# Kernel tuning notes

Hardware: AMD Instinct MI355X
Metric: run time of the kernel (lower is better)

The kernel has to match this reference:

```python
import jax, jax.numpy as jnp
import numpy as np

N = 100000   # nodes
E = 1600000  # edges
G = 512      # graphs
L = 3        # num_unit LEConv layers
D = 64       # hidden dim


def setup_inputs() -> dict:
    key = jax.random.key(0)
    ks = jax.random.split(key, 12)
    s = 1.0 / np.sqrt(D)
    x = jax.random.normal(ks[0], (N, 4), jnp.float32)
    edge_index = jax.random.randint(ks[1], (2, E), 0, N, dtype=jnp.int64)
    edge_attr = jax.random.uniform(ks[2], (E,), jnp.float32)
    batch = jnp.sort(jax.random.randint(ks[3], (N,), 0, G, dtype=jnp.int64))
    return {
        "x": x,
        "edge_index": edge_index,
        "edge_attr": edge_attr,
        "batch": batch,
        "W_emb": jax.random.normal(ks[4], (4, D), jnp.float32) * 0.5,
        "b_emb": jnp.zeros((D,), jnp.float32),
        "W1": jax.random.normal(ks[5], (L, D, D), jnp.float32) * s,  # LEConv lin1 (on x_j)
        "b1": jnp.zeros((L, D), jnp.float32),
        "W2": jax.random.normal(ks[6], (L, D, D), jnp.float32) * s,  # LEConv lin2 (on x_i, no bias)
        "W3": jax.random.normal(ks[7], (L, D, D), jnp.float32) * s,  # LEConv lin3 (root)
        "b3": jnp.zeros((L, D), jnp.float32),
        "Wl1": jax.random.normal(ks[8], (D, 32), jnp.float32) * s,
        "bl1": jnp.zeros((32,), jnp.float32),
        "Wl2": jax.random.normal(ks[9], (32, 3), jnp.float32) * (1.0 / np.sqrt(32)),
        "bl2": jnp.zeros((3,), jnp.float32),
    }


def reference(x, edge_index, edge_attr, batch, W_emb, b_emb,
              W1, b1, W2, W3, b3, Wl1, bl1, Wl2, bl2):
    src, dst = edge_index[0], edge_index[1]
    h = x @ W_emb + b_emb                          # [N, D]
    for l in range(L):
        a = h @ W1[l] + b1[l]                      # lin1(x) -> gathered at source j
        b = h @ W2[l]                              # lin2(x) -> gathered at target i
        # LEConv message: e_ij * (lin1(x_j) - lin2(x_i)), aggr='add' at target
        msg = edge_attr[:, None] * (a[src] - b[dst])   # [E, D]
        agg = jax.ops.segment_sum(msg, dst, num_segments=N)
        h = jax.nn.relu(agg + h @ W3[l] + b3[l])
    # global_mean_pool over graphs
    sums = jax.ops.segment_sum(h, batch, num_segments=G)              # [G, D]
    counts = jax.ops.segment_sum(jnp.ones((N,), h.dtype), batch, num_segments=G)
    graph_x = sums / jnp.maximum(counts, 1.0)[:, None]
    pred = jax.nn.relu(graph_x @ Wl1 + bl1) @ Wl2 + bl2               # [G, 3]
    return pred
```

## Files before the change

### kernel.cpp

```cpp
#include <hip/hip_runtime.h>
#include <hip/hip_bf16.h>

#define NNODES 100000
#define NEDGES 1600000
#define NGRAPH 512
#define DIM    64
#define NLAYER 3

#define NB   1000
#define BN   100
#define CAP  2048
#define SC_BLOCKS 256
#define EPB  6250
#define PACK_BLOCKS 18
#define ZERO_BLOCKS 2
#define NBLK32 3125
#define EMB_BLOCKS 6250

typedef __attribute__((ext_vector_type(8))) short short8;
typedef __attribute__((ext_vector_type(4))) float float4v;
typedef unsigned long long u64;

__device__ __forceinline__ __hip_bfloat16 f2b(float f) { return __float2bfloat16(f); }
__device__ __forceinline__ unsigned short f2b_bits(float f) {
    __hip_bfloat16 h = __float2bfloat16(f);
    return *reinterpret_cast<unsigned short*>(&h);
}

__device__ __forceinline__ unsigned pack_rec(int src, unsigned wbits32) {
    unsigned w15 = ((wbits32 + 0x8000u) >> 16) & 0x7FFFu;
    return ((unsigned)src << 15) | w15;
}

#define ACC4(ACC, RR, VV) do {                                              \
    float _w = __uint_as_float(((RR) & 0x7FFFu) << 16);                     \
    unsigned _lo = (unsigned)(VV), _hi = (unsigned)((VV) >> 32);            \
    ACC[0] = fmaf(_w, __uint_as_float(_lo << 16), ACC[0]);                  \
    ACC[1] = fmaf(_w, __uint_as_float(_lo & 0xFFFF0000u), ACC[1]);          \
    ACC[2] = fmaf(_w, __uint_as_float(_hi << 16), ACC[2]);                  \
    ACC[3] = fmaf(_w, __uint_as_float(_hi & 0xFFFF0000u), ACC[3]);          \
} while (0)

__device__ __forceinline__ void gather_rounds(
    unsigned rec, int cnt, const u64* __restrict__ h64, int q, int p,
    float (&accA)[4], float (&accB)[4], float (&accC)[4], float (&accD)[4]) {
    int full = cnt >> 4;
    for (int t = 0; t < full; ++t) {
        int base = t * 16;
        unsigned rA = (unsigned)__shfl((int)rec, base + q, 64);
        unsigned rB = (unsigned)__shfl((int)rec, base + 4 + q, 64);
        unsigned rC = (unsigned)__shfl((int)rec, base + 8 + q, 64);
        unsigned rD = (unsigned)__shfl((int)rec, base + 12 + q, 64);
        u64 vA = h64[(size_t)(rA >> 15) * 16 + p];
        u64 vB = h64[(size_t)(rB >> 15) * 16 + p];
        u64 vC = h64[(size_t)(rC >> 15) * 16 + p];
        u64 vD = h64[(size_t)(rD >> 15) * 16 + p];
        ACC4(accA, rA, vA);
        ACC4(accB, rB, vB);
        ACC4(accC, rC, vC);
        ACC4(accD, rD, vD);
    }
    int rem = cnt & 15;
    if (rem) {
        int base = full << 4;
        unsigned rA = (unsigned)__shfl((int)rec, base + q, 64);
        u64 vA = h64[(size_t)(rA >> 15) * 16 + p];
        unsigned rB = 0u, rC = 0u, rD = 0u;
        u64 vB = 0, vC = 0, vD = 0;
        if (rem > 4) {
            rB = (unsigned)__shfl((int)rec, base + 4 + q, 64);
            vB = h64[(size_t)(rB >> 15) * 16 + p];
        }
        if (rem > 8) {
            rC = (unsigned)__shfl((int)rec, base + 8 + q, 64);
            vC = h64[(size_t)(rC >> 15) * 16 + p];
        }
        if (rem > 12) {
            rD = (unsigned)__shfl((int)rec, base + 12 + q, 64);
            vD = h64[(size_t)(rD >> 15) * 16 + p];
        }
        ACC4(accA, rA, vA);
        ACC4(accB, rB, vB);
        ACC4(accC, rC, vC);
        ACC4(accD, rD, vD);
    }
}


__global__ __launch_bounds__(256) void local_sort_kernel(
    const int* __restrict__ ei, const float* __restrict__ ea,
    int2* __restrict__ perm_raw, int2* __restrict__ offcnt,
    const float* __restrict__ W1, const float* __restrict__ W2,
    const float* __restrict__ W3, __hip_bfloat16* __restrict__ wpack,
    float* __restrict__ gsum) {
    int tid = threadIdx.x, k = blockIdx.x;
    if (k >= SC_BLOCKS + PACK_BLOCKS) {
        float4v z = {0.f, 0.f, 0.f, 0.f};
        int idx = (k - SC_BLOCKS - PACK_BLOCKS) * 256 + tid;
        for (int i = idx; i < NGRAPH * DIM / 4; i += ZERO_BLOCKS * 256)
            ((float4v*)gsum)[i] = z;
        return;
    }
    if (k >= SC_BLOCKS) {
        int unit = (k - SC_BLOCKS) * 4 + (tid >> 6);
        if (unit < NLAYER * 24) {
            int kh = unit & 1, tn = (unit >> 1) & 3, w = (unit >> 3) % 3, l = unit / 24;
            const float* Wsrc = (w == 0 ? W1 : (w == 1 ? W2 : W3)) + l * 4096;
            int L = tid & 63;
            __hip_bfloat16* dst = wpack + (size_t)unit * 512 + L * 8;
            int kb = 32 * kh + (L >> 4) * 8;
            int nb = 16 * tn + (L & 15);
            #pragma unroll
            for (int j = 0; j < 8; ++j)
                dst[j] = f2b(Wsrc[(kb + j) * 64 + nb]);
        }
        return;
    }
    __shared__ int cnt[NB];
    __shared__ int off[NB];
    __shared__ int partial[256];
    __shared__ int2 srec[EPB];
    int e0 = k * EPB;
    for (int i = tid; i < NB; i += 256) cnt[i] = 0;
    __syncthreads();
    for (int i = tid; i < EPB; i += 256)
        atomicAdd(&cnt[ei[NEDGES + e0 + i] / BN], 1);
    __syncthreads();
    int loc[4]; int s = 0;
    #pragma unroll
    for (int j = 0; j < 4; ++j) {
        int b = tid * 4 + j;
        int v = (b < NB) ? cnt[b] : 0;
        loc[j] = s; s += v;
    }
    partial[tid] = s;
    __syncthreads();
    for (int o = 1; o < 256; o <<= 1) {
        int t = (tid >= o) ? partial[tid - o] : 0;
        __syncthreads();
        partial[tid] += t;
        __syncthreads();
    }
    int excl = partial[tid] - s;
    #pragma unroll
    for (int j = 0; j < 4; ++j) {
        int b = tid * 4 + j;
        if (b < NB) off[b] = excl + loc[j];
    }
    __syncthreads();
    for (int b = tid; b < NB; b += 256)
        offcnt[(size_t)k * NB + b] = make_int2(off[b], cnt[b]);
    __syncthreads();
    for (int i = tid; i < EPB; i += 256) {
        int e = e0 + i;
        int src = ei[e];
        int d = ei[NEDGES + e];
        float w = ea[e];
        int bin = d / BN;
        int dloc = d - bin * BN;
        int pos = atomicAdd(&off[bin], 1);
        srec[pos] = make_int2(src | (dloc << 20), __float_as_int(w));
    }
    __syncthreads();
    for (int i = tid; i < EPB; i += 256)
        perm_raw[e0 + i] = srec[i];
}

__global__ __launch_bounds__(256) void csr_embed_kernel(
    const int2* __restrict__ perm_raw, const int2* __restrict__ offcnt,
    unsigned* __restrict__ perm2, int2* __restrict__ rows, float* __restrict__ wdeg,
    const float* __restrict__ x, const float* __restrict__ Wemb,
    const float* __restrict__ bemb, __hip_bfloat16* __restrict__ h) {
    __shared__ int2     recs[CAP];
    __shared__ unsigned recs2u[CAP];
    __shared__ int   pscan[256];
    __shared__ int   sprefix[SC_BLOCKS + 1];
    __shared__ int   boff[SC_BLOCKS];
    __shared__ int   cnt[BN];
    __shared__ int   start[BN];
    __shared__ int   cur[BN];
    __shared__ float ws[BN];
    int b = blockIdx.x, tid = threadIdx.x;
    if (b >= NB) {
        int t = (b - NB) * 256 + tid;
        int node = t >> 4, d0 = (t & 15) * 4;
        float4v xv = *(const float4v*)&x[(size_t)node * 4];
        u64 w0 = 0;
        #pragma unroll
        for (int j = 0; j < 4; ++j) {
            int ch = d0 + j;
            float s = bemb[ch];
            #pragma unroll
            for (int k = 0; k < 4; ++k) s = fmaf(xv[k], Wemb[k * 64 + ch], s);
            w0 |= (u64)f2b_bits(s) << (16 * j);
        }
        ((u64*)h)[(size_t)node * 16 + (t & 15)] = w0;
        return;
    }
    if (tid < BN) { cnt[tid] = 0; ws[tid] = 0.f; }
    int2 oc = offcnt[(size_t)tid * NB + b];
    boff[tid] = oc.x;
    int c = oc.y;
    pscan[tid] = c;
    __syncthreads();
    for (int o = 1; o < 256; o <<= 1) {
        int t = (tid >= o) ? pscan[tid - o] : 0;
        __syncthreads();
        pscan[tid] += t;
        __syncthreads();
    }
    sprefix[tid] = pscan[tid] - c;
    if (tid == 255) sprefix[256] = pscan[255];
    __syncthreads();
    int n = min(sprefix[SC_BLOCKS], CAP);
    for (int i = tid; i < n; i += 256) {
        int lo = 0, hi = SC_BLOCKS;
        while (hi - lo > 1) { int m = (lo + hi) >> 1; if (sprefix[m] <= i) lo = m; else hi = m; }
        int2 rec = perm_raw[lo * EPB + boff[lo] + (i - sprefix[lo])];
        recs[i] = rec;
        atomicAdd(&cnt[rec.x >> 20], 1);
        atomicAdd(&ws[rec.x >> 20], __int_as_float(rec.y));
    }
    __syncthreads();
    {
        int v = (tid < BN) ? cnt[tid] : 0;
        pscan[tid] = v;
        __syncthreads();
        for (int o = 1; o < 128; o <<= 1) {
            int t = (tid >= o) ? pscan[tid - o] : 0;
            __syncthreads();
            pscan[tid] += t;
            __syncthreads();
        }
        if (tid < BN) start[tid] = pscan[tid] - v;
    }
    __syncthreads();
    if (tid < BN) {
        cur[tid] = start[tid];
        int base = b * CAP + start[tid];
        rows[b * BN + tid] = make_int2(base, base + cnt[tid]);
        wdeg[b * BN + tid] = ws[tid];
    }
    __syncthreads();
    for (int i = tid; i < n; i += 256) {
        int2 rec = recs[i];
        int pos = atomicAdd(&cur[rec.x >> 20], 1);
        recs2u[pos] = pack_rec(rec.x & 0xFFFFF, (unsigned)rec.y);
    }
    __syncthreads();
    for (int i = tid; i < n; i += 256)
        perm2[(size_t)b * CAP + i] = recs2u[i];
}


template <int LAST>
__global__ __launch_bounds__(256, 8) void layer_kernel(
    const __hip_bfloat16* __restrict__ hin, __hip_bfloat16* __restrict__ hout,
    const int2* __restrict__ rows, const unsigned* __restrict__ perm2,
    const float* __restrict__ wdeg, const __hip_bfloat16* __restrict__ wpack,
    const float* __restrict__ b1, const float* __restrict__ b3,
    const int* __restrict__ batch, float* __restrict__ gsum) {
    __shared__ __align__(16) unsigned char mbytes[32 * 128];
    int tid = threadIdx.x;
    int lane = tid & 63, wv = tid >> 6;
    int q = lane >> 4, p = lane & 15;
    int m0 = blockIdx.x * 32 + wv * 8;
    const u64* h64 = (const u64*)hin;

    int2 rl = rows[m0 + (lane & 7)];
    int st_n = __shfl(rl.x, 0, 64);
    int en_n = __shfl(rl.y, 0, 64);
    unsigned rec_n = (lane < min(en_n - st_n, 64)) ? perm2[st_n + lane] : 0u;

    for (int nl = 0; nl < 8; ++nl) {
        int st = st_n, en = en_n;
        unsigned rec = rec_n;
        if (nl < 7) {
            st_n = __shfl(rl.x, nl + 1, 64);
            en_n = __shfl(rl.y, nl + 1, 64);
            rec_n = (lane < min(en_n - st_n, 64)) ? perm2[st_n + lane] : 0u;
        }
        float accA[4] = {0.f, 0.f, 0.f, 0.f};
        float accB[4] = {0.f, 0.f, 0.f, 0.f};
        float accC[4] = {0.f, 0.f, 0.f, 0.f};
        float accD[4] = {0.f, 0.f, 0.f, 0.f};
        gather_rounds(rec, min(en - st, 64), h64, q, p, accA, accB, accC, accD);
        for (int cb = st + 64; cb < en; cb += 64) {
            unsigned rec2 = (lane < en - cb) ? perm2[cb + lane] : 0u;
            gather_rounds(rec2, min(en - cb, 64), h64, q, p, accA, accB, accC, accD);
        }
        #pragma unroll
        for (int j = 0; j < 4; ++j) accA[j] = (accA[j] + accB[j]) + (accC[j] + accD[j]);
        #pragma unroll
        for (int j = 0; j < 4; ++j) accA[j] += __shfl_xor(accA[j], 16, 64);
        #pragma unroll
        for (int j = 0; j < 4; ++j) accA[j] += __shfl_xor(accA[j], 32, 64);
        if (q == 0) {
            u64 w0 = (u64)f2b_bits(accA[0]) | ((u64)f2b_bits(accA[1]) << 16) |
                     ((u64)f2b_bits(accA[2]) << 32) | ((u64)f2b_bits(accA[3]) << 48);
            int row = wv * 8 + nl;
            int off = (row * 128 + p * 8) ^ ((row & 7) << 4);
            *(u64*)(mbytes + off) = w0;
        }
    }
    __syncthreads();
    if (wv >= 2) return;

    float4v acc[3][4] = {};
    const short8* wp = (const short8*)wpack;
    int row = wv * 16 + p;
    int node_c = blockIdx.x * 32 + row;
    #pragma unroll
    for (int kh = 0; kh < 2; ++kh) {
        int roff = (row * 128 + kh * 64 + q * 16) ^ ((row & 7) << 4);
        short8 am = *(const short8*)(mbytes + roff);
        short8 ah = *(const short8*)((const short*)hin + (size_t)node_c * 64 + kh * 32 + q * 8);
        #pragma unroll
        for (int w = 0; w < 3; ++w) {
            #pragma unroll
            for (int tn = 0; tn < 4; ++tn) {
                short8 bfrag = wp[(size_t)((w * 4 + tn) * 2 + kh) * 64 + lane];
                acc[w][tn] = __builtin_amdgcn_mfma_f32_16x16x32_bf16(
                    w == 0 ? am : ah, bfrag, acc[w][tn], 0, 0, 0);
            }
        }
    }

    float b1v[4], b3v[4];
    #pragma unroll
    for (int tn = 0; tn < 4; ++tn) {
        b1v[tn] = b1[tn * 16 + p];
        b3v[tn] = b3[tn * 16 + p];
    }
    int tb = blockIdx.x * 32 + wv * 16;
    if (!LAST) {
        #pragma unroll
        for (int reg = 0; reg < 4; ++reg) {
            int node = tb + q * 4 + reg;
            float wd = wdeg[node];
            #pragma unroll
            for (int tn = 0; tn < 4; ++tn) {
                float s = acc[0][tn][reg] + acc[2][tn][reg] + b3v[tn] +
                          wd * (b1v[tn] - acc[1][tn][reg]);
                hout[(size_t)node * 64 + tn * 16 + p] = f2b(fmaxf(s, 0.f));
            }
        }
    } else {
        float val[4][4];
        int gb[4];
        #pragma unroll
        for (int reg = 0; reg < 4; ++reg) {
            int node = tb + q * 4 + reg;
            float wd = wdeg[node];
            gb[reg] = batch[node];
            #pragma unroll
            for (int tn = 0; tn < 4; ++tn) {
                float s = acc[0][tn][reg] + acc[2][tn][reg] + b3v[tn] +
                          wd * (b1v[tn] - acc[1][tn][reg]);
                val[reg][tn] = fmaxf(s, 0.f);
            }
        }
        int glo = batch[tb];
        int ghi = batch[tb + 15];
        for (int g = glo; g <= ghi; ++g) {
            #pragma unroll
            for (int tn = 0; tn < 4; ++tn) {
                float part = 0.f;
                #pragma unroll
                for (int reg = 0; reg < 4; ++reg)
                    part += (gb[reg] == g) ? val[reg][tn] : 0.f;
                part += __shfl_xor(part, 16, 64);
                part += __shfl_xor(part, 32, 64);
                if (q == 0) atomicAdd(&gsum[g * 64 + tn * 16 + p], part);
            }
        }
    }
}


__global__ __launch_bounds__(64) void mlp_kernel(
    const float* __restrict__ gsum, const int* __restrict__ batch,
    const float* __restrict__ Wl1, const float* __restrict__ bl1,
    const float* __restrict__ Wl2, const float* __restrict__ bl2,
    float* __restrict__ out) {
    __shared__ int lohi[2];
    __shared__ float gxl[64];
    __shared__ float hid[32];
    int g = blockIdx.x, t = threadIdx.x;
    if (t < 2) {
        int target = g + t;
        int lo = 0, hi = NNODES;
        while (lo < hi) { int m = (lo + hi) >> 1; if (batch[m] < target) lo = m + 1; else hi = m; }
        lohi[t] = lo;
    }
    __syncthreads();
    int cnt = lohi[1] - lohi[0];
    gxl[t] = gsum[g * 64 + t] / (float)max(cnt, 1);
    __syncthreads();
    if (t < 32) {
        float s = bl1[t];
        for (int k = 0; k < 64; ++k) s = fmaf(gxl[k], Wl1[k * 32 + t], s);
        hid[t] = fmaxf(s, 0.f);
    }
    __syncthreads();
    if (t < 3) {
        float s = bl2[t];
        for (int k = 0; k < 32; ++k) s = fmaf(hid[k], Wl2[k * 3 + t], s);
        out[g * 3 + t] = s;
    }
}


extern "C" void kernel_launch(void* const* d_in, const int* in_sizes, int n_in,
                              void* d_out, int out_size, void* d_ws, size_t ws_size,
                              hipStream_t stream) {
    const float* x    = (const float*)d_in[0];
    const int*   ei   = (const int*)d_in[1];
    const float* ea   = (const float*)d_in[2];
    const int*   bat  = (const int*)d_in[3];
    const float* Wemb = (const float*)d_in[4];
    const float* bemb = (const float*)d_in[5];
    const float* W1   = (const float*)d_in[6];
    const float* b1   = (const float*)d_in[7];
    const float* W2   = (const float*)d_in[8];
    const float* W3   = (const float*)d_in[9];
    const float* b3   = (const float*)d_in[10];
    const float* Wl1  = (const float*)d_in[11];
    const float* bl1  = (const float*)d_in[12];
    const float* Wl2  = (const float*)d_in[13];
    const float* bl2  = (const float*)d_in[14];
    float* out = (float*)d_out;

    char* ws = (char*)d_ws;
    __hip_bfloat16*  h_b      = (__hip_bfloat16*) (ws + 0);
    __hip_bfloat16*  h_a      = (__hip_bfloat16*) (ws + 12800000);
    int2*            perm_raw = (int2*)           (ws + 25600000);
    unsigned*        perm2    = (unsigned*)       (ws + 38400000);
    int2*            rows     = (int2*)           (ws + 46592000);
    int2*            offcnt   = (int2*)           (ws + 47392000);
    float*           wdeg     = (float*)          (ws + 49440000);
    __hip_bfloat16*  wpack    = (__hip_bfloat16*) (ws + 49840000);
    float*           gsum     = (float*)          (ws + 49913728);

    local_sort_kernel<<<SC_BLOCKS + PACK_BLOCKS + ZERO_BLOCKS, 256, 0, stream>>>(
        ei, ea, perm_raw, offcnt, W1, W2, W3, wpack, gsum);
    csr_embed_kernel<<<NB + EMB_BLOCKS, 256, 0, stream>>>(
        perm_raw, offcnt, perm2, rows, wdeg, x, Wemb, bemb, h_a);

    layer_kernel<0><<<NBLK32, 256, 0, stream>>>(
        h_a, h_b, rows, perm2, wdeg, wpack, b1, b3, bat, gsum);
    layer_kernel<0><<<NBLK32, 256, 0, stream>>>(
        h_b, h_a, rows, perm2, wdeg, wpack + (size_t)24 * 512, b1 + 64, b3 + 64, bat, gsum);
    layer_kernel<1><<<NBLK32, 256, 0, stream>>>(
        h_a, h_b, rows, perm2, wdeg, wpack + (size_t)48 * 512, b1 + 128, b3 + 128, bat, gsum);

    mlp_kernel<<<NGRAPH, 64, 0, stream>>>(gsum, bat, Wl1, bl1, Wl2, bl2, out);
}
```

Baseline: 268.2 us.

## Load edge records per round directly and split MFMA epilogue across all four waves

The gather loop no longer preloads up to 64 edge records per node and broadcasts them with shuffles. Each 16-edge round now loads its four records straight from perm2, with bounds masks. The dense MFMA stage used to run on only two waves; it now splits the output columns so all four waves each compute two of the four 16-column tiles, and the hidden-state stores become nontemporal. This is meant to cut shuffle overhead, shorten the serial epilogue and use idle waves. In exchange, every wave reloads the A fragments, and the record loads now sit on the critical path before the dependent gathers, since the next node's prefetch is gone.

```diff
diff --git a/kernel.cpp b/kernel.cpp
--- a/kernel.cpp
+++ b/kernel.cpp
@@ -40,51 +40,6 @@
     ACC[2] = fmaf(_w, __uint_as_float(_hi << 16), ACC[2]);                  \
     ACC[3] = fmaf(_w, __uint_as_float(_hi & 0xFFFF0000u), ACC[3]);          \
 } while (0)
-
-__device__ __forceinline__ void gather_rounds(
-    unsigned rec, int cnt, const u64* __restrict__ h64, int q, int p,
-    float (&accA)[4], float (&accB)[4], float (&accC)[4], float (&accD)[4]) {
-    int full = cnt >> 4;
-    for (int t = 0; t < full; ++t) {
-        int base = t * 16;
-        unsigned rA = (unsigned)__shfl((int)rec, base + q, 64);
-        unsigned rB = (unsigned)__shfl((int)rec, base + 4 + q, 64);
-        unsigned rC = (unsigned)__shfl((int)rec, base + 8 + q, 64);
-        unsigned rD = (unsigned)__shfl((int)rec, base + 12 + q, 64);
-        u64 vA = h64[(size_t)(rA >> 15) * 16 + p];
-        u64 vB = h64[(size_t)(rB >> 15) * 16 + p];
-        u64 vC = h64[(size_t)(rC >> 15) * 16 + p];
-        u64 vD = h64[(size_t)(rD >> 15) * 16 + p];
-        ACC4(accA, rA, vA);
-        ACC4(accB, rB, vB);
-        ACC4(accC, rC, vC);
-        ACC4(accD, rD, vD);
-    }
-    int rem = cnt & 15;
-    if (rem) {
-        int base = full << 4;
-        unsigned rA = (unsigned)__shfl((int)rec, base + q, 64);
-        u64 vA = h64[(size_t)(rA >> 15) * 16 + p];
-        unsigned rB = 0u, rC = 0u, rD = 0u;
-        u64 vB = 0, vC = 0, vD = 0;
-        if (rem > 4) {
-            rB = (unsigned)__shfl((int)rec, base + 4 + q, 64);
-            vB = h64[(size_t)(rB >> 15) * 16 + p];
-        }
-        if (rem > 8) {
-            rC = (unsigned)__shfl((int)rec, base + 8 + q, 64);
-            vC = h64[(size_t)(rC >> 15) * 16 + p];
-        }
-        if (rem > 12) {
-            rD = (unsigned)__shfl((int)rec, base + 12 + q, 64);
-            vD = h64[(size_t)(rD >> 15) * 16 + p];
-        }
-        ACC4(accA, rA, vA);
-        ACC4(accB, rB, vB);
-        ACC4(accC, rC, vC);
-        ACC4(accD, rD, vD);
-    }
-}
 
 
 __global__ __launch_bounds__(256) void local_sort_kernel(
@@ -264,30 +219,33 @@
     int tid = threadIdx.x;
     int lane = tid & 63, wv = tid >> 6;
     int q = lane >> 4, p = lane & 15;
-    int m0 = blockIdx.x * 32 + wv * 8;
+    int n0 = blockIdx.x * 32 + wv * 8;
     const u64* h64 = (const u64*)hin;
 
-    int2 rl = rows[m0 + (lane & 7)];
-    int st_n = __shfl(rl.x, 0, 64);
-    int en_n = __shfl(rl.y, 0, 64);
-    unsigned rec_n = (lane < min(en_n - st_n, 64)) ? perm2[st_n + lane] : 0u;
-
+    #pragma unroll
     for (int nl = 0; nl < 8; ++nl) {
-        int st = st_n, en = en_n;
-        unsigned rec = rec_n;
-        if (nl < 7) {
-            st_n = __shfl(rl.x, nl + 1, 64);
-            en_n = __shfl(rl.y, nl + 1, 64);
-            rec_n = (lane < min(en_n - st_n, 64)) ? perm2[st_n + lane] : 0u;
-        }
+        int2 rl = rows[n0 + nl];
+        int st = rl.x, en = rl.y;
         float accA[4] = {0.f, 0.f, 0.f, 0.f};
         float accB[4] = {0.f, 0.f, 0.f, 0.f};
         float accC[4] = {0.f, 0.f, 0.f, 0.f};
         float accD[4] = {0.f, 0.f, 0.f, 0.f};
-        gather_rounds(rec, min(en - st, 64), h64, q, p, accA, accB, accC, accD);
-        for (int cb = st + 64; cb < en; cb += 64) {
-            unsigned rec2 = (lane < en - cb) ? perm2[cb + lane] : 0u;
-            gather_rounds(rec2, min(en - cb, 64), h64, q, p, accA, accB, accC, accD);
+        for (int i0 = st; i0 < en; i0 += 16) {
+            int iA = i0 + q, iB = i0 + 4 + q, iC = i0 + 8 + q, iD = i0 + 12 + q;
+            unsigned rA = 0u, rB = 0u, rC = 0u, rD = 0u;
+            if (iA < en) rA = perm2[iA];
+            if (iB < en) rB = perm2[iB];
+            if (iC < en) rC = perm2[iC];
+            if (iD < en) rD = perm2[iD];
+            u64 vA = 0, vB = 0, vC = 0, vD = 0;
+            if (iA < en) vA = h64[(size_t)(rA >> 15) * 16 + p];
+            if (iB < en) vB = h64[(size_t)(rB >> 15) * 16 + p];
+            if (iC < en) vC = h64[(size_t)(rC >> 15) * 16 + p];
+            if (iD < en) vD = h64[(size_t)(rD >> 15) * 16 + p];
+            ACC4(accA, rA, vA);
+            ACC4(accB, rB, vB);
+            ACC4(accC, rC, vC);
+            ACC4(accD, rD, vD);
         }
         #pragma unroll
         for (int j = 0; j < 4; ++j) accA[j] = (accA[j] + accB[j]) + (accC[j] + accD[j]);
@@ -304,11 +262,11 @@
         }
     }
     __syncthreads();
-    if (wv >= 2) return;
-
-    float4v acc[3][4] = {};
+
+    int tile = wv >> 1, ch = wv & 1;
+    float4v acc[3][2] = {};
     const short8* wp = (const short8*)wpack;
-    int row = wv * 16 + p;
+    int row = tile * 16 + p;
     int node_c = blockIdx.x * 32 + row;
     #pragma unroll
     for (int kh = 0; kh < 2; ++kh) {
@@ -318,35 +276,40 @@
         #pragma unroll
         for (int w = 0; w < 3; ++w) {
             #pragma unroll
-            for (int tn = 0; tn < 4; ++tn) {
+            for (int t = 0; t < 2; ++t) {
+                int tn = ch * 2 + t;
                 short8 bfrag = wp[(size_t)((w * 4 + tn) * 2 + kh) * 64 + lane];
-                acc[w][tn] = __builtin_amdgcn_mfma_f32_16x16x32_bf16(
-                    w == 0 ? am : ah, bfrag, acc[w][tn], 0, 0, 0);
+                acc[w][t] = __builtin_amdgcn_mfma_f32_16x16x32_bf16(
+                    w == 0 ? am : ah, bfrag, acc[w][t], 0, 0, 0);
             }
         }
     }
 
-    float b1v[4], b3v[4];
+    float b1v[2], b3v[2];
     #pragma unroll
-    for (int tn = 0; tn < 4; ++tn) {
-        b1v[tn] = b1[tn * 16 + p];
-        b3v[tn] = b3[tn * 16 + p];
-    }
-    int tb = blockIdx.x * 32 + wv * 16;
+    for (int t = 0; t < 2; ++t) {
+        int tn = ch * 2 + t;
+        b1v[t] = b1[tn * 16 + p];
+        b3v[t] = b3[tn * 16 + p];
+    }
+    int tb = blockIdx.x * 32 + tile * 16;
     if (!LAST) {
+        unsigned short* hout_u = (unsigned short*)hout;
         #pragma unroll
         for (int reg = 0; reg < 4; ++reg) {
             int node = tb + q * 4 + reg;
             float wd = wdeg[node];
             #pragma unroll
-            for (int tn = 0; tn < 4; ++tn) {
-                float s = acc[0][tn][reg] + acc[2][tn][reg] + b3v[tn] +
-                          wd * (b1v[tn] - acc[1][tn][reg]);
-                hout[(size_t)node * 64 + tn * 16 + p] = f2b(fmaxf(s, 0.f));
+            for (int t = 0; t < 2; ++t) {
+                int tn = ch * 2 + t;
+                float s = acc[0][t][reg] + acc[2][t][reg] + b3v[t] +
+                          wd * (b1v[t] - acc[1][t][reg]);
+                __builtin_nontemporal_store(f2b_bits(fmaxf(s, 0.f)),
+                                            &hout_u[(size_t)node * 64 + tn * 16 + p]);
             }
         }
     } else {
-        float val[4][4];
+        float val[4][2];
         int gb[4];
         #pragma unroll
         for (int reg = 0; reg < 4; ++reg) {
@@ -354,21 +317,22 @@
             float wd = wdeg[node];
             gb[reg] = batch[node];
             #pragma unroll
-            for (int tn = 0; tn < 4; ++tn) {
-                float s = acc[0][tn][reg] + acc[2][tn][reg] + b3v[tn] +
-                          wd * (b1v[tn] - acc[1][tn][reg]);
-                val[reg][tn] = fmaxf(s, 0.f);
+            for (int t = 0; t < 2; ++t) {
+                float s = acc[0][t][reg] + acc[2][t][reg] + b3v[t] +
+                          wd * (b1v[t] - acc[1][t][reg]);
+                val[reg][t] = fmaxf(s, 0.f);
             }
         }
         int glo = batch[tb];
         int ghi = batch[tb + 15];
         for (int g = glo; g <= ghi; ++g) {
             #pragma unroll
-            for (int tn = 0; tn < 4; ++tn) {
+            for (int t = 0; t < 2; ++t) {
+                int tn = ch * 2 + t;
                 float part = 0.f;
                 #pragma unroll
                 for (int reg = 0; reg < 4; ++reg)
-                    part += (gb[reg] == g) ? val[reg][tn] : 0.f;
+                    part += (gb[reg] == g) ? val[reg][t] : 0.f;
                 part += __shfl_xor(part, 16, 64);
                 part += __shfl_xor(part, 32, 64);
                 if (q == 0) atomicAdd(&gsum[g * 64 + tn * 16 + p], part);
```

Result: slower. 310.2 us (+15.6%).
